# Kernel optimization log

Measured on AMD Instinct MI355X. Metric: run time of the kernel, lower is better.

The kernel has to match this reference:

```python
import jax, jax.numpy as jnp
import numpy as np

N = 8192
IN_CH = 512
HID = 256
OUT_CH = 64
AVG_DEG = 16
BN_EPS = 1e-5


def _build_adjs():
    """Replicates H2GCN.init_adj: 1-hop adj (no self loops) and strict 2-hop adj,
    both symmetrically gcn-normalized (D^-1/2 A D^-1/2, no self loops)."""
    rng = np.random.default_rng(0)
    col = rng.integers(0, N, size=(N, AVG_DEG))
    A = np.zeros((N, N), dtype=np.float32)
    A[np.repeat(np.arange(N), AVG_DEG), col.ravel()] = 1.0
    A = np.maximum(A, A.T)               # undirected
    np.fill_diagonal(A, 0.0)             # remove_diag
    A2 = (A @ A > 0).astype(np.float32)  # 2-hop reachability
    A2 = A2 * (1.0 - A)                  # strict two-hop: subtract 1-hop edges
    np.fill_diagonal(A2, 0.0)

    def gcn_norm(M):
        d = M.sum(axis=1)
        dis = np.where(d > 0, 1.0 / np.sqrt(np.maximum(d, 1e-12)), 0.0).astype(np.float32)
        return dis[:, None] * M * dis[None, :]

    return gcn_norm(A), gcn_norm(A2)


def setup_inputs() -> dict:
    key = jax.random.key(0)
    k = jax.random.split(key, 4)
    adj_t, adj_t2 = _build_adjs()
    return {
        "x": jax.random.normal(k[0], (N, IN_CH), dtype=jnp.float32),
        "adj_t": jnp.asarray(adj_t),
        "adj_t2": jnp.asarray(adj_t2),
        "w_embed": jax.random.normal(k[1], (HID, IN_CH), dtype=jnp.float32) / np.sqrt(IN_CH),
        "b_embed": jnp.zeros((HID,), dtype=jnp.float32),
        "bn_gamma": jnp.ones((2 * HID,), dtype=jnp.float32),
        "bn_beta": jnp.zeros((2 * HID,), dtype=jnp.float32),
        "w_fin": jax.random.normal(k[2], (OUT_CH, 7 * HID), dtype=jnp.float32) / np.sqrt(7 * HID),
        "b_fin": jnp.zeros((OUT_CH,), dtype=jnp.float32),
    }


def reference(x, adj_t, adj_t2, w_embed, b_embed, bn_gamma, bn_beta, w_fin, b_fin):
    # feature_embed: single Linear (num_mlp_layers=1), then ReLU activation
    h = jax.nn.relu(x @ w_embed.T + b_embed)            # [n, h]
    xs = [h]
    # conv 1: concat(A @ h, A2 @ h), then BatchNorm1d (batch statistics)
    z = jnp.concatenate([adj_t @ h, adj_t2 @ h], axis=1)  # [n, 2h]
    mean = jnp.mean(z, axis=0)
    var = jnp.var(z, axis=0)
    z = (z - mean) * jax.lax.rsqrt(var + BN_EPS) * bn_gamma + bn_beta
    xs.append(z)
    # conv 2 (last conv, no BN)
    z2 = jnp.concatenate([adj_t @ z, adj_t2 @ z], axis=1)  # [n, 4h]
    xs.append(z2)
    # JumpingKnowledge('cat') + final projection: [n, 7h] -> [n, out]
    jk = jnp.concatenate(xs, axis=1)
    return jk @ w_fin.T + b_fin
```

## Files before the change

kernel.cpp:

```cpp
#include <hip/hip_runtime.h>
#include <stdint.h>

typedef unsigned long long u64;

#define NR   8192
#define INC  512
#define HID  256
#define OUTC 64
#define NW   128
#define BN_EPS 1e-5f
#define NZBUF 1152

static constexpr size_t OFF_H    = 0;
static constexpr size_t OFF_Z    = OFF_H    + (size_t)NR*HID*4;
static constexpr size_t OFF_PQ   = OFF_Z    + (size_t)NR*2*HID*4;
static constexpr size_t OFF_BMP  = OFF_PQ   + (size_t)NR*128*4;
static constexpr size_t OFF_DIS  = OFF_BMP  + (size_t)2*NR*NW*8;
static constexpr size_t OFF_SUM  = OFF_DIS  + (size_t)2*NR*4;
static constexpr size_t OFF_SSQ  = OFF_SUM  + (size_t)2*HID*4;
static constexpr size_t WS_NEED  = OFF_SSQ  + (size_t)2*HID*4;

__global__ void extract_bitmap(const float* __restrict__ A, const float* __restrict__ A2,
                               u64* __restrict__ words, float* __restrict__ dis) {
    const int r    = blockIdx.x;
    const int mat  = blockIdx.y;
    const int tid  = threadIdx.x;
    const int lane = tid & 63;
    const int wv   = tid >> 6;
    __shared__ int scnt;
    if (tid == 0) scnt = 0;
    __syncthreads();
    const float* rowp = (mat ? A2 : A) + (size_t)r * NR;
    u64* wout = words + ((size_t)mat * NR + r) * NW;
    int myc = 0;
    for (int w = wv; w < NW; w += 4) {
        float v = rowp[w * 64 + lane];
        u64 m = __ballot(v != 0.0f);
        if (lane == 0) {
            wout[w] = m;
            myc += __popcll(m);
        }
    }
    if (lane == 0) atomicAdd(&scnt, myc);
    __syncthreads();
    if (tid == 0) {
        int c = scnt;
        dis[mat * NR + r] = (c > 0) ? (float)(1.0 / sqrt((double)c)) : 0.0f;
    }
}

__global__ void gemm_embed(const float* __restrict__ X, const float* __restrict__ W,
                           const float* __restrict__ B, float* __restrict__ H) {
    __shared__ __align__(16) float sA[16][68];
    __shared__ __align__(16) float sB[16][68];
    const int m0 = blockIdx.x * 64, n0 = blockIdx.y * 64;
    const int tid = threadIdx.x;
    const int tx = tid & 15, ty = tid >> 4;
    float acc[4][4] = {};
    for (int kt = 0; kt < INC; kt += 16) {
        for (int e = tid; e < 64 * 16; e += 256) {
            int row = e >> 4, k = e & 15;
            sA[k][row] = X[(size_t)(m0 + row) * INC + kt + k];
            sB[k][row] = W[(size_t)(n0 + row) * INC + kt + k];
        }
        __syncthreads();
#pragma unroll
        for (int k = 0; k < 16; ++k) {
            float4 av = *(const float4*)&sA[k][ty * 4];
            float4 bv = *(const float4*)&sB[k][tx * 4];
            float a[4] = {av.x, av.y, av.z, av.w};
            float b[4] = {bv.x, bv.y, bv.z, bv.w};
#pragma unroll
            for (int i = 0; i < 4; ++i)
#pragma unroll
                for (int j = 0; j < 4; ++j) acc[i][j] = fmaf(a[i], b[j], acc[i][j]);
        }
        __syncthreads();
    }
#pragma unroll
    for (int i = 0; i < 4; ++i)
#pragma unroll
        for (int j = 0; j < 4; ++j) {
            int m = m0 + ty * 4 + i, n = n0 + tx * 4 + j;
            H[(size_t)m * HID + n] = fmaxf(acc[i][j] + B[n], 0.0f);
        }
}

template <int WSRC, int VEC>
__device__ void spmm_phase(const u64* __restrict__ wp, int w0, int nw,
                           const float* __restrict__ disc, const float* __restrict__ src,
                           int j, uint2* s_nz, int* s_off, float* acc) {
    const int tid = threadIdx.x;
    __syncthreads();
    u64 m = 0;
    if (tid < nw) {
        m = wp[w0 + tid];
        s_off[tid] = __popcll(m);
    }
    __syncthreads();
    if (tid < 64) {
        int cnt_i = (tid < nw) ? s_off[tid] : 0;
        int v = cnt_i;
#pragma unroll
        for (int d = 1; d < 64; d <<= 1) {
            int t = __shfl_up(v, d, 64);
            if (tid >= d) v += t;
        }
        if (tid < nw) s_off[tid] = v - cnt_i;
        if (tid == 63) s_off[64] = v;
    }
    __syncthreads();
    const int total = s_off[64];
    if (tid < nw) {
        int o = s_off[tid];
        u64 mm = m;
        while (mm) {
            int b = __builtin_ctzll(mm);
            mm &= mm - 1;
            int c = (w0 + tid) * 64 + b;
            s_nz[o] = make_uint2((unsigned)c, __float_as_uint(disc[c]));
            ++o;
        }
    }
    __syncthreads();
#pragma unroll 4
    for (int k = 0; k < total; ++k) {
        uint2 p = s_nz[k];
        float val = __uint_as_float(p.y);
        const float* sp = &src[(size_t)p.x * WSRC + VEC * j];
        if constexpr (VEC == 2) {
            float2 v = *(const float2*)sp;
            acc[0] = fmaf(val, v.x, acc[0]);
            acc[1] = fmaf(val, v.y, acc[1]);
        } else {
            float4 v = *(const float4*)sp;
            acc[0] = fmaf(val, v.x, acc[0]);
            acc[1] = fmaf(val, v.y, acc[1]);
            acc[2] = fmaf(val, v.z, acc[2]);
            acc[3] = fmaf(val, v.w, acc[3]);
        }
    }
}

template <int WSRC, int VEC, int NPHASE>
__global__ __launch_bounds__(128, 8)
void spmm_kernel(const u64* __restrict__ bmp, const float* __restrict__ dis,
                 const float* __restrict__ src, float* __restrict__ dst) {
    const int r = blockIdx.x;
    const int j = threadIdx.x;
    __shared__ uint2 s_nz[NZBUF];
    __shared__ int s_off[65];
    const u64* wpA = bmp + (size_t)r * NW;
    const u64* wpB = bmp + (size_t)(NR + r) * NW;
    const float* disA = dis;
    const float* disB = dis + NR;
    float accA[VEC] = {}, accB[VEC] = {};
    const int WPP = NW / NPHASE;
    for (int ph = 0; ph < NPHASE; ++ph) {
        int w0 = ph * WPP;
        spmm_phase<WSRC, VEC>(wpA, w0, WPP, disA, src, j, s_nz, s_off, accA);
        spmm_phase<WSRC, VEC>(wpB, w0, WPP, disB, src, j, s_nz, s_off, accB);
    }
    const float da = disA[r], db = disB[r];
#pragma unroll
    for (int q = 0; q < VEC; ++q) {
        dst[(size_t)r * 2 * WSRC + VEC * j + q]        = da * accA[q];
        dst[(size_t)r * 2 * WSRC + WSRC + VEC * j + q] = db * accB[q];
    }
}

__global__ void zero_stats(float* __restrict__ gsum, float* __restrict__ gssq) {
    int i = blockIdx.x * 256 + threadIdx.x;
    if (i < 2 * HID) gsum[i] = 0.0f;
    else if (i < 4 * HID) gssq[i - 2 * HID] = 0.0f;
}

__global__ void bn_stats(const float* __restrict__ Z, float* __restrict__ gsum,
                         float* __restrict__ gssq) {
    const int tid = threadIdx.x;
    const int cl = tid & 63, rg = tid >> 6;
    const int c = blockIdx.x * 64 + cl;
    const int r0 = blockIdx.y * 128 + rg * 32;
    float s = 0.0f, s2 = 0.0f;
    for (int i = 0; i < 32; ++i) {
        float v = Z[(size_t)(r0 + i) * (2 * HID) + c];
        s += v;
        s2 += v * v;
    }
    __shared__ float red[2][4][64];
    red[0][rg][cl] = s;
    red[1][rg][cl] = s2;
    __syncthreads();
    if (tid < 64) {
        float t0 = red[0][0][tid] + red[0][1][tid] + red[0][2][tid] + red[0][3][tid];
        float t1 = red[1][0][tid] + red[1][1][tid] + red[1][2][tid] + red[1][3][tid];
        atomicAdd(&gsum[blockIdx.x * 64 + tid], t0);
        atomicAdd(&gssq[blockIdx.x * 64 + tid], t1);
    }
}

__global__ void bn_apply(float* __restrict__ Z, const float* __restrict__ gsum,
                         const float* __restrict__ gssq, const float* __restrict__ gamma,
                         const float* __restrict__ beta) {
    const size_t idx = (size_t)blockIdx.x * 256 + threadIdx.x;
    const int c = (int)(idx & (2 * HID - 1));
    const float inv = 1.0f / (float)NR;
    float mean = gsum[c] * inv;
    float var = fmaxf(gssq[c] * inv - mean * mean, 0.0f);
    float rs = rsqrtf(var + BN_EPS);
    Z[idx] = (Z[idx] - mean) * rs * gamma[c] + beta[c];
}

__global__ void gemm_pq(const float* __restrict__ Z, const float* __restrict__ WF,
                        float* __restrict__ PQ) {
    __shared__ __align__(16) float sA[16][36];
    __shared__ __align__(16) float sB[16][132];
    const int m0 = blockIdx.x * 32;
    const int tid = threadIdx.x;
    const int tx = tid & 31, ty = tid >> 5;
    float acc[4][4] = {};
    for (int kt = 0; kt < 2 * HID; kt += 16) {
        for (int e = tid; e < 32 * 16; e += 256) {
            int row = e >> 4, k = e & 15;
            sA[k][row] = Z[(size_t)(m0 + row) * (2 * HID) + kt + k];
        }
        for (int e = tid; e < 128 * 16; e += 256) {
            int n = e >> 4, k = e & 15;
            int col = (n < 64) ? (3 * HID + kt + k) : (5 * HID + kt + k);
            sB[k][n] = WF[(size_t)(n & 63) * (7 * HID) + col];
        }
        __syncthreads();
#pragma unroll
        for (int k = 0; k < 16; ++k) {
            float4 av = *(const float4*)&sA[k][ty * 4];
            float4 bv = *(const float4*)&sB[k][tx * 4];
            float a[4] = {av.x, av.y, av.z, av.w};
            float b[4] = {bv.x, bv.y, bv.z, bv.w};
#pragma unroll
            for (int i = 0; i < 4; ++i)
#pragma unroll
                for (int j = 0; j < 4; ++j) acc[i][j] = fmaf(a[i], b[j], acc[i][j]);
        }
        __syncthreads();
    }
#pragma unroll
    for (int i = 0; i < 4; ++i)
#pragma unroll
        for (int j = 0; j < 4; ++j) {
            int m = m0 + ty * 4 + i, n = tx * 4 + j;
            PQ[(size_t)m * 128 + n] = acc[i][j];
        }
}

__global__ void gemm_final(const float* __restrict__ H, const float* __restrict__ Z,
                           const float* __restrict__ WF, const float* __restrict__ B,
                           float* __restrict__ OUT) {
    __shared__ __align__(16) float sA[16][36];
    __shared__ __align__(16) float sB[16][68];
    const int m0 = blockIdx.x * 32;
    const int tid = threadIdx.x;
    const int tx = tid & 15, ty = tid >> 4;
    float acc[4][4] = {};
    for (int kt = 0; kt < 3 * HID; kt += 16) {
        const float* src;
        int stride, koff;
        if (kt < HID) { src = H; stride = HID;     koff = kt; }
        else          { src = Z; stride = 2 * HID; koff = kt - HID; }
        for (int e = tid; e < 32 * 16; e += 128) {
            int row = e >> 4, k = e & 15;
            sA[k][row] = src[(size_t)(m0 + row) * stride + koff + k];
        }
        for (int e = tid; e < 64 * 16; e += 128) {
            int row = e >> 4, k = e & 15;
            sB[k][row] = WF[(size_t)row * (7 * HID) + kt + k];
        }
        __syncthreads();
#pragma unroll
        for (int k = 0; k < 16; ++k) {
            float4 av = *(const float4*)&sA[k][ty * 4];
            float4 bv = *(const float4*)&sB[k][tx * 4];
            float a[4] = {av.x, av.y, av.z, av.w};
            float b[4] = {bv.x, bv.y, bv.z, bv.w};
#pragma unroll
            for (int i = 0; i < 4; ++i)
#pragma unroll
                for (int j = 0; j < 4; ++j) acc[i][j] = fmaf(a[i], b[j], acc[i][j]);
        }
        __syncthreads();
    }
#pragma unroll
    for (int i = 0; i < 4; ++i)
#pragma unroll
        for (int j = 0; j < 4; ++j) {
            int m = m0 + ty * 4 + i, n = tx * 4 + j;
            OUT[(size_t)m * OUTC + n] = acc[i][j] + B[n];
        }
}

__device__ int decode64(const u64* __restrict__ wp, int w0,
                        const float* __restrict__ disc, uint2* s_nz, int* s_off) {
    const int tid = threadIdx.x;
    u64 m = 0;
    if (tid < 64) {
        m = wp[w0 + tid];
        s_off[tid] = __popcll(m);
    }
    __syncthreads();
    if (tid < 64) {
        int cnt_i = s_off[tid];
        int v = cnt_i;
#pragma unroll
        for (int d = 1; d < 64; d <<= 1) {
            int t = __shfl_up(v, d, 64);
            if (tid >= d) v += t;
        }
        s_off[tid] = v - cnt_i;
        if (tid == 63) s_off[64] = v;
    }
    __syncthreads();
    int total = s_off[64];
    if (tid < 64) {
        int o = s_off[tid];
        u64 mm = m;
        while (mm) {
            int b = __builtin_ctzll(mm);
            mm &= mm - 1;
            int c = (w0 + tid) * 64 + b;
            s_nz[o] = make_uint2((unsigned)c, __float_as_uint(disc[c]));
            ++o;
        }
    }
    __syncthreads();
    return total;
}

__global__ __launch_bounds__(128, 8)
void spmm_pq(const u64* __restrict__ bmp, const float* __restrict__ dis,
             const float* __restrict__ PQ, float* __restrict__ OUT) {
    const int r = blockIdx.x;
    const int tid = threadIdx.x;
    const int j = tid & 63, half = tid >> 6;
    __shared__ uint2 s_nzA[128];
    __shared__ uint2 s_nzB[NZBUF];
    __shared__ int s_off[65];
    __shared__ float s_res[128];
    const u64* wpA = bmp + (size_t)r * NW;
    const u64* wpB = bmp + (size_t)(NR + r) * NW;
    const float* disA = dis;
    const float* disB = dis + NR;
    float accA = 0.0f, accB = 0.0f;
    for (int ph = 0; ph < 2; ++ph) {
        __syncthreads();
        int w0 = ph * 64;
        int totA = decode64(wpA, w0, disA, s_nzA, s_off);
        int totB = decode64(wpB, w0, disB, s_nzB, s_off);
        int midB = (totB + 1) >> 1;
        if (half == 0) {
            for (int k = 0; k < totA; ++k) {
                uint2 p = s_nzA[k];
                accA = fmaf(__uint_as_float(p.y), PQ[(size_t)p.x * 128 + j], accA);
            }
        }
        int b0 = half ? midB : 0;
        int b1 = half ? totB : midB;
#pragma unroll 4
        for (int k = b0; k < b1; ++k) {
            uint2 p = s_nzB[k];
            accB = fmaf(__uint_as_float(p.y), PQ[(size_t)p.x * 128 + 64 + j], accB);
        }
    }
    s_res[tid] = accB;
    __syncthreads();
    if (tid < 64) {
        float add = disA[r] * accA + disB[r] * (s_res[tid] + s_res[tid + 64]);
        OUT[(size_t)r * OUTC + tid] += add;
    }
}

extern "C" void kernel_launch(void* const* d_in, const int* in_sizes, int n_in,
                              void* d_out, int out_size, void* d_ws, size_t ws_size,
                              hipStream_t stream) {
    const float* x     = (const float*)d_in[0];
    const float* adj   = (const float*)d_in[1];
    const float* adj2  = (const float*)d_in[2];
    const float* w_emb = (const float*)d_in[3];
    const float* b_emb = (const float*)d_in[4];
    const float* gamma = (const float*)d_in[5];
    const float* beta  = (const float*)d_in[6];
    const float* w_fin = (const float*)d_in[7];
    const float* b_fin = (const float*)d_in[8];
    float* out = (float*)d_out;

    if (ws_size < WS_NEED) return;

    char* ws = (char*)d_ws;
    float* h    = (float*)(ws + OFF_H);
    float* z    = (float*)(ws + OFF_Z);
    float* pq   = (float*)(ws + OFF_PQ);
    u64*   bmp  = (u64*)  (ws + OFF_BMP);
    float* dis  = (float*)(ws + OFF_DIS);
    float* gsum = (float*)(ws + OFF_SUM);
    float* gssq = (float*)(ws + OFF_SSQ);

    extract_bitmap<<<dim3(NR, 2), 256, 0, stream>>>(adj, adj2, bmp, dis);

    gemm_embed<<<dim3(NR / 64, HID / 64), 256, 0, stream>>>(x, w_emb, b_emb, h);

    spmm_kernel<HID, 2, 4><<<NR, HID / 2, 0, stream>>>(bmp, dis, h, z);

    zero_stats<<<4, 256, 0, stream>>>(gsum, gssq);
    bn_stats<<<dim3(8, 64), 256, 0, stream>>>(z, gsum, gssq);
    bn_apply<<<(NR * 2 * HID) / 256, 256, 0, stream>>>(z, gsum, gssq, gamma, beta);

    gemm_pq<<<NR / 32, 256, 0, stream>>>(z, w_fin, pq);

    gemm_final<<<NR / 32, 128, 0, stream>>>(h, z, w_fin, b_fin, out);

    spmm_pq<<<NR, 128, 0, stream>>>(bmp, dis, pq, out);
}
```

Measured before the change: 1.509 ms.

## Split SpMM into per-column-range launches for L2 locality of gathered rows

The fused SpMM kernel, which looped over four column-word ranges inside each block, becomes four separate launches. In each launch every block gathers source rows from only one quarter of the node range, so the working set can stay cache-resident. The final PQ SpMM is likewise split into two launches that accumulate into the output. Row-side degree scaling moves out of the SpMM into bn_stats and bn_apply, and neighbour indices are pre-multiplied into byte offsets to save address arithmetic. The cost is extra launches and repeated read-modify-write passes over the intermediate z and output buffers.

```diff
diff --git a/kernel.cpp b/kernel.cpp
--- a/kernel.cpp
+++ b/kernel.cpp
@@ -88,8 +88,8 @@
 
 template <int WSRC, int VEC>
 __device__ void spmm_phase(const u64* __restrict__ wp, int w0, int nw,
-                           const float* __restrict__ disc, const float* __restrict__ src,
-                           int j, uint2* s_nz, int* s_off, float* acc) {
+                           const float* __restrict__ disc, const char* __restrict__ sbase,
+                           uint2* s_nz, int* s_off, float* acc) {
     const int tid = threadIdx.x;
     __syncthreads();
     u64 m = 0;
@@ -118,7 +118,7 @@
             int b = __builtin_ctzll(mm);
             mm &= mm - 1;
             int c = (w0 + tid) * 64 + b;
-            s_nz[o] = make_uint2((unsigned)c, __float_as_uint(disc[c]));
+            s_nz[o] = make_uint2((unsigned)(c * (WSRC * 4)), __float_as_uint(disc[c]));
             ++o;
         }
     }
@@ -127,7 +127,7 @@
     for (int k = 0; k < total; ++k) {
         uint2 p = s_nz[k];
         float val = __uint_as_float(p.y);
-        const float* sp = &src[(size_t)p.x * WSRC + VEC * j];
+        const float* sp = (const float*)(sbase + p.x);
         if constexpr (VEC == 2) {
             float2 v = *(const float2*)sp;
             acc[0] = fmaf(val, v.x, acc[0]);
@@ -142,30 +142,24 @@
     }
 }
 
-template <int WSRC, int VEC, int NPHASE>
+template <int WSRC, int VEC, int NWP, bool FIRST>
 __global__ __launch_bounds__(128, 8)
-void spmm_kernel(const u64* __restrict__ bmp, const float* __restrict__ dis,
-                 const float* __restrict__ src, float* __restrict__ dst) {
+void spmm_phase_acc(const u64* __restrict__ bmp, const float* __restrict__ dis,
+                    const float* __restrict__ src, float* __restrict__ dst, int w0) {
     const int r = blockIdx.x;
     const int j = threadIdx.x;
     __shared__ uint2 s_nz[NZBUF];
     __shared__ int s_off[65];
-    const u64* wpA = bmp + (size_t)r * NW;
-    const u64* wpB = bmp + (size_t)(NR + r) * NW;
-    const float* disA = dis;
-    const float* disB = dis + NR;
     float accA[VEC] = {}, accB[VEC] = {};
-    const int WPP = NW / NPHASE;
-    for (int ph = 0; ph < NPHASE; ++ph) {
-        int w0 = ph * WPP;
-        spmm_phase<WSRC, VEC>(wpA, w0, WPP, disA, src, j, s_nz, s_off, accA);
-        spmm_phase<WSRC, VEC>(wpB, w0, WPP, disB, src, j, s_nz, s_off, accB);
-    }
-    const float da = disA[r], db = disB[r];
+    const char* sbase = (const char*)src + (size_t)(VEC * 4) * j;
+    spmm_phase<WSRC, VEC>(bmp + (size_t)r * NW,        w0, NWP, dis,      sbase, s_nz, s_off, accA);
+    spmm_phase<WSRC, VEC>(bmp + (size_t)(NR + r) * NW, w0, NWP, dis + NR, sbase, s_nz, s_off, accB);
 #pragma unroll
     for (int q = 0; q < VEC; ++q) {
-        dst[(size_t)r * 2 * WSRC + VEC * j + q]        = da * accA[q];
-        dst[(size_t)r * 2 * WSRC + WSRC + VEC * j + q] = db * accB[q];
+        float* pa = &dst[(size_t)r * 2 * WSRC + VEC * j + q];
+        float* pb = &dst[(size_t)r * 2 * WSRC + WSRC + VEC * j + q];
+        if constexpr (FIRST) { *pa = accA[q];  *pb = accB[q]; }
+        else                 { *pa += accA[q]; *pb += accB[q]; }
     }
 }
 
@@ -175,15 +169,16 @@
     else if (i < 4 * HID) gssq[i - 2 * HID] = 0.0f;
 }
 
-__global__ void bn_stats(const float* __restrict__ Z, float* __restrict__ gsum,
-                         float* __restrict__ gssq) {
+__global__ void bn_stats(const float* __restrict__ Z, const float* __restrict__ dis,
+                         float* __restrict__ gsum, float* __restrict__ gssq) {
     const int tid = threadIdx.x;
     const int cl = tid & 63, rg = tid >> 6;
     const int c = blockIdx.x * 64 + cl;
     const int r0 = blockIdx.y * 128 + rg * 32;
+    const float* drow = (blockIdx.x < 4) ? dis : dis + NR;
     float s = 0.0f, s2 = 0.0f;
     for (int i = 0; i < 32; ++i) {
-        float v = Z[(size_t)(r0 + i) * (2 * HID) + c];
+        float v = Z[(size_t)(r0 + i) * (2 * HID) + c] * drow[r0 + i];
         s += v;
         s2 += v * v;
     }
@@ -199,16 +194,18 @@
     }
 }
 
-__global__ void bn_apply(float* __restrict__ Z, const float* __restrict__ gsum,
-                         const float* __restrict__ gssq, const float* __restrict__ gamma,
-                         const float* __restrict__ beta) {
+__global__ void bn_apply(float* __restrict__ Z, const float* __restrict__ dis,
+                         const float* __restrict__ gsum, const float* __restrict__ gssq,
+                         const float* __restrict__ gamma, const float* __restrict__ beta) {
     const size_t idx = (size_t)blockIdx.x * 256 + threadIdx.x;
     const int c = (int)(idx & (2 * HID - 1));
+    const int r = (int)(idx >> 9);
+    const float sc = ((c < HID) ? dis : dis + NR)[r];
     const float inv = 1.0f / (float)NR;
     float mean = gsum[c] * inv;
     float var = fmaxf(gssq[c] * inv - mean * mean, 0.0f);
     float rs = rsqrtf(var + BN_EPS);
-    Z[idx] = (Z[idx] - mean) * rs * gamma[c] + beta[c];
+    Z[idx] = (Z[idx] * sc - mean) * rs * gamma[c] + beta[c];
 }
 
 __global__ void gemm_pq(const float* __restrict__ Z, const float* __restrict__ WF,
@@ -326,7 +323,7 @@
             int b = __builtin_ctzll(mm);
             mm &= mm - 1;
             int c = (w0 + tid) * 64 + b;
-            s_nz[o] = make_uint2((unsigned)c, __float_as_uint(disc[c]));
+            s_nz[o] = make_uint2((unsigned)(c * 512), __float_as_uint(disc[c]));
             ++o;
         }
     }
@@ -336,7 +333,7 @@
 
 __global__ __launch_bounds__(128, 8)
 void spmm_pq(const u64* __restrict__ bmp, const float* __restrict__ dis,
-             const float* __restrict__ PQ, float* __restrict__ OUT) {
+             const float* __restrict__ PQ, float* __restrict__ OUT, int w0) {
     const int r = blockIdx.x;
     const int tid = threadIdx.x;
     const int j = tid & 63, half = tid >> 6;
@@ -344,30 +341,26 @@
     __shared__ uint2 s_nzB[NZBUF];
     __shared__ int s_off[65];
     __shared__ float s_res[128];
-    const u64* wpA = bmp + (size_t)r * NW;
-    const u64* wpB = bmp + (size_t)(NR + r) * NW;
     const float* disA = dis;
     const float* disB = dis + NR;
     float accA = 0.0f, accB = 0.0f;
-    for (int ph = 0; ph < 2; ++ph) {
-        __syncthreads();
-        int w0 = ph * 64;
-        int totA = decode64(wpA, w0, disA, s_nzA, s_off);
-        int totB = decode64(wpB, w0, disB, s_nzB, s_off);
-        int midB = (totB + 1) >> 1;
-        if (half == 0) {
-            for (int k = 0; k < totA; ++k) {
-                uint2 p = s_nzA[k];
-                accA = fmaf(__uint_as_float(p.y), PQ[(size_t)p.x * 128 + j], accA);
-            }
-        }
-        int b0 = half ? midB : 0;
-        int b1 = half ? totB : midB;
+    int totA = decode64(bmp + (size_t)r * NW,        w0, disA, s_nzA, s_off);
+    __syncthreads();
+    int totB = decode64(bmp + (size_t)(NR + r) * NW, w0, disB, s_nzB, s_off);
+    const char* base = (const char*)PQ + 4 * j;
+    int midB = (totB + 1) >> 1;
+    if (half == 0) {
+        for (int k = 0; k < totA; ++k) {
+            uint2 p = s_nzA[k];
+            accA = fmaf(__uint_as_float(p.y), *(const float*)(base + p.x), accA);
+        }
+    }
+    int b0 = half ? midB : 0;
+    int b1 = half ? totB : midB;
 #pragma unroll 4
-        for (int k = b0; k < b1; ++k) {
-            uint2 p = s_nzB[k];
-            accB = fmaf(__uint_as_float(p.y), PQ[(size_t)p.x * 128 + 64 + j], accB);
-        }
+    for (int k = b0; k < b1; ++k) {
+        uint2 p = s_nzB[k];
+        accB = fmaf(__uint_as_float(p.y), *(const float*)(base + 256 + p.x), accB);
     }
     s_res[tid] = accB;
     __syncthreads();
@@ -406,15 +399,19 @@
 
     gemm_embed<<<dim3(NR / 64, HID / 64), 256, 0, stream>>>(x, w_emb, b_emb, h);
 
-    spmm_kernel<HID, 2, 4><<<NR, HID / 2, 0, stream>>>(bmp, dis, h, z);
+    spmm_phase_acc<HID, 2, 32, true ><<<NR, 128, 0, stream>>>(bmp, dis, h, z, 0);
+    spmm_phase_acc<HID, 2, 32, false><<<NR, 128, 0, stream>>>(bmp, dis, h, z, 32);
+    spmm_phase_acc<HID, 2, 32, false><<<NR, 128, 0, stream>>>(bmp, dis, h, z, 64);
+    spmm_phase_acc<HID, 2, 32, false><<<NR, 128, 0, stream>>>(bmp, dis, h, z, 96);
 
     zero_stats<<<4, 256, 0, stream>>>(gsum, gssq);
-    bn_stats<<<dim3(8, 64), 256, 0, stream>>>(z, gsum, gssq);
-    bn_apply<<<(NR * 2 * HID) / 256, 256, 0, stream>>>(z, gsum, gssq, gamma, beta);
+    bn_stats<<<dim3(8, 64), 256, 0, stream>>>(z, dis, gsum, gssq);
+    bn_apply<<<(NR * 2 * HID) / 256, 256, 0, stream>>>(z, dis, gsum, gssq, gamma, beta);
 
     gemm_pq<<<NR / 32, 256, 0, stream>>>(z, w_fin, pq);
 
     gemm_final<<<NR / 32, 128, 0, stream>>>(h, z, w_fin, b_fin, out);
 
-    spmm_pq<<<NR, 128, 0, stream>>>(bmp, dis, pq, out);
-}
+    spmm_pq<<<NR, 128, 0, stream>>>(bmp, dis, pq, out, 0);
+    spmm_pq<<<NR, 128, 0, stream>>>(bmp, dis, pq, out, 64);
+}
```

After: 1.492 ms. Within noise of the previous version (-1.1%).
